# Kernel tuning notes

Measured on AMD Instinct MI355X. Metric: run time of the kernel, lower is better.

Reference implementation:

```python
import jax, jax.numpy as jnp
import numpy as np

# Lattice / model constants (from init_kwargs)
LX, LY = 12, 12
N = LX * LY
NH = 64              # GRU hidden units
K = 2                # local Hilbert-space dim (occupied / empty)
NSAMPLES = 4096
EPS = 1e-10


def setup_inputs() -> dict:
    key = jax.random.key(0)
    k1, k2, k3 = jax.random.split(key, 3)
    s_in = 1.0 / np.sqrt(K + NH)   # glorot-ish scale for input kernel
    s_rec = 1.0 / np.sqrt(NH)
    W = (jax.random.normal(k1, (K, 3 * NH)) * s_in).astype(jnp.float32)    # GRU input kernel
    U = (jax.random.normal(k2, (NH, 3 * NH)) * s_rec).astype(jnp.float32)  # GRU recurrent kernel
    b = jnp.zeros((2, 3 * NH), dtype=jnp.float32)   # reset_after: [input_bias, recurrent_bias]
    Wd = (jax.random.normal(k3, (NH, K)) * s_rec).astype(jnp.float32)      # Dense kernel
    bd = jnp.zeros((K,), dtype=jnp.float32)
    return {"nsamples": NSAMPLES, "W": W, "U": U, "b": b, "Wd": Wd, "bd": bd}


def _gru_cell(x, h, W, U, b):
    # TF2 Keras GRU cell, reset_after=True, tanh / sigmoid activations.
    xm = x @ W + b[0]                      # [ns, 3nh]
    hm = h @ U + b[1]                      # [ns, 3nh]
    xz, xr, xn = jnp.split(xm, 3, axis=1)
    hz, hr, hn = jnp.split(hm, 3, axis=1)
    z = jax.nn.sigmoid(xz + hz)            # update gate
    r = jax.nn.sigmoid(xr + hr)            # reset gate
    hh = jnp.tanh(xn + r * hn)             # candidate
    return z * h + (1.0 - z) * hh


def reference(nsamples, W, U, b, Wd, bd):
    keys = jax.random.split(jax.random.key(42), N)
    h0 = jnp.zeros((nsamples, NH), dtype=W.dtype)
    x0 = jnp.zeros((nsamples, K), dtype=W.dtype)   # 0.0 * one_hot(0)
    logP0 = jnp.zeros((nsamples,), dtype=W.dtype)

    def step(carry, k):
        h, x, logP = carry
        h = _gru_cell(x, h, W, U, b)
        probs = jax.nn.softmax(h @ Wd + bd, axis=-1)     # Dense with softmax activation
        logp = jnp.log(EPS + probs)                      # [ns, K]
        s = jax.random.categorical(k, logp, axis=-1)     # [ns] int sample
        x_new = jax.nn.one_hot(s, K, dtype=W.dtype)
        logP = logP + jnp.sum(logp * x_new, axis=1)
        return (h, x_new, logP), s

    (_, _, logP), samples = jax.lax.scan(step, (h0, x0, logP0), keys)
    samples = samples.T                                  # [ns, N]
    return samples, logP
```

## Files before the change

### kernel.cpp

```cpp
#include <hip/hip_runtime.h>
#include <cstdint>
#include <math.h>


#define NSAMP 4096
#define NSTEP 144
#define HID 64
#define CPB 2

typedef float v16f __attribute__((ext_vector_type(16)));
typedef float v4f  __attribute__((ext_vector_type(4)));
typedef float v2f  __attribute__((ext_vector_type(2)));

__device__ __forceinline__ void threefry2x32(uint32_t k0, uint32_t k1,
                                             uint32_t x0, uint32_t x1,
                                             uint32_t& o0, uint32_t& o1) {
  const uint32_t ks0 = k0, ks1 = k1, ks2 = k0 ^ k1 ^ 0x1BD11BDAu;
  x0 += ks0; x1 += ks1;
#define TF_ROUND(d) { x0 += x1; x1 = (x1 << (d)) | (x1 >> (32 - (d))); x1 ^= x0; }
  TF_ROUND(13) TF_ROUND(15) TF_ROUND(26) TF_ROUND(6)
  x0 += ks1; x1 += ks2 + 1u;
  TF_ROUND(17) TF_ROUND(29) TF_ROUND(16) TF_ROUND(24)
  x0 += ks2; x1 += ks0 + 2u;
  TF_ROUND(13) TF_ROUND(15) TF_ROUND(26) TF_ROUND(6)
  x0 += ks0; x1 += ks1 + 3u;
  TF_ROUND(17) TF_ROUND(29) TF_ROUND(16) TF_ROUND(24)
  x0 += ks1; x1 += ks2 + 4u;
  TF_ROUND(13) TF_ROUND(15) TF_ROUND(26) TF_ROUND(6)
  x0 += ks2; x1 += ks0 + 5u;
#undef TF_ROUND
  o0 = x0; o1 = x1;
}

__device__ __forceinline__ float fsig(float x) {
  return __builtin_amdgcn_rcpf(1.0f + __expf(-x));
}
__device__ __forceinline__ float ftanh(float x) {
  const float e = __expf(2.0f * x);
  return 1.0f - 2.0f * __builtin_amdgcn_rcpf(e + 1.0f);
}

#define PKFMA_LO(acc, h2, up) \
  asm("v_pk_fma_f32 %0, %1, %2, %0 op_sel_hi:[1,0,1]" \
      : "+v"(acc) : "v"(h2), "v"(up));
#define PKFMA_HI(acc, h2, up) \
  asm("v_pk_fma_f32 %0, %1, %2, %0 op_sel:[0,1,0] op_sel_hi:[1,1,1]" \
      : "+v"(acc) : "v"(h2), "v"(up));

template <int CTRL>
__device__ __forceinline__ float dpp_add(float v) {
  union { float f; int i; } c; c.f = v;
  union { int i; float f; } r;
  r.i = __builtin_amdgcn_mov_dpp(c.i, CTRL, 0xF, 0xF, true);
  return v + r.f;
}
#define DPP_XOR1 0xB1
#define DPP_XOR2 0x4E
#define DPP_XOR4 0x141
#define DPP_XOR8 0x140

__global__ __launch_bounds__(64, 1) void vmc_kernel(
    const float* __restrict__ W, const float* __restrict__ U,
    const float* __restrict__ B, const float* __restrict__ Wd,
    const float* __restrict__ Bd, float* __restrict__ out) {
  const int j = threadIdx.x;
  const int s_base = blockIdx.x * CPB;

  __shared__ __align__(16) float2 hsh2[HID];
  __shared__ uint2 kkeys[NSTEP];
  __shared__ float gsh[CPB * 2 * NSTEP];

#pragma unroll 1
  for (int t = j; t < NSTEP; t += HID) {
    uint32_t o0, o1;
    threefry2x32(0u, 42u, 0u, (uint32_t)t, o0, o1);
    kkeys[t].x = o0; kkeys[t].y = o1;
  }
  hsh2[j] = float2{0.0f, 0.0f};
  __syncthreads();

#pragma unroll 1
  for (int id = j; id < CPB * 2 * NSTEP; id += HID) {
    const int c = id / 288;
    const int idx = id - c * 288;
    const uint2 kt = kkeys[idx >> 1];
    const uint32_t i = 2u * (uint32_t)(s_base + c) + (uint32_t)(idx & 1);
    uint32_t o0, o1;
    threefry2x32(kt.x, kt.y, 0u, i, o0, o1);
    const uint32_t bits = o0 ^ o1;
    union { uint32_t u; float f; } cv; cv.u = (bits >> 9) | 0x3F800000u;
    float uf = cv.f - 1.0f;
    uf = fmaxf(uf, 1.17549435e-38f);
    const float inner = (float)log((double)uf);
    gsh[id] = -(float)log((double)(-inner));
  }
  __syncthreads();

  v16f uz0, uz1, uz2, uz3, ur0, ur1, ur2, ur3, un0, un1, un2, un3;
#define LOADB(v, r, off) \
  { _Pragma("unroll") for (int e = 0; e < 16; ++e) v[e] = U[((r)*16 + e)*192 + (off) + j]; }
  LOADB(uz0, 0, 0)    LOADB(uz1, 1, 0)    LOADB(uz2, 2, 0)    LOADB(uz3, 3, 0)
  LOADB(ur0, 0, 64)   LOADB(ur1, 1, 64)   LOADB(ur2, 2, 64)   LOADB(ur3, 3, 64)
  LOADB(un0, 0, 128)  LOADB(un1, 1, 128)  LOADB(un2, 2, 128)  LOADB(un3, 3, 128)
#undef LOADB

  const float b1z = B[192 + j], b1r = B[256 + j], b1n = B[320 + j];
  const float b0z = B[j],       b0r = B[64 + j],  b0n = B[128 + j];
  const float xW0z = W[j]       + b0z, xW1z = W[192 + j] + b0z;
  const float xW0r = W[64 + j]  + b0r, xW1r = W[256 + j] + b0r;
  const float xW0n = W[128 + j] + b0n, xW1n = W[320 + j] + b0n;
  const float wdd = Wd[2*j + 1] - Wd[2*j];
  const float bdd = Bd[1] - Bd[0];

  float ha = 0.0f, hb_ = 0.0f;
  float logPa = 0.0f, logPb = 0.0f;
  float axz = b0z, axr = b0r, axn = b0n;
  float bxz = b0z, bxr = b0r, bxn = b0n;
  v2f hz2 = {0.f, 0.f}, hr2 = {0.f, 0.f}, hn2 = {0.f, 0.f};

  for (int t = 0; t < NSTEP; ++t) {
    {
      const float az = axz + (hz2.x + b1z), ar = axr + (hr2.x + b1r);
      const float zz = fsig(az), rr = fsig(ar);
      const float hh = ftanh(axn + rr * (hn2.x + b1n));
      ha = zz * ha + (1.0f - zz) * hh;
    }
    {
      const float az = bxz + (hz2.y + b1z), ar = bxr + (hr2.y + b1r);
      const float zz = fsig(az), rr = fsig(ar);
      const float hh = ftanh(bxn + rr * (hn2.y + b1n));
      hb_ = zz * hb_ + (1.0f - zz) * hh;
    }
    hsh2[j] = float2{ha, hb_};

    float da = ha * wdd, db = hb_ * wdd;
    da = dpp_add<DPP_XOR1>(da); db = dpp_add<DPP_XOR1>(db);
    da = dpp_add<DPP_XOR2>(da); db = dpp_add<DPP_XOR2>(db);
    da = dpp_add<DPP_XOR4>(da); db = dpp_add<DPP_XOR4>(db);
    da = dpp_add<DPP_XOR8>(da); db = dpp_add<DPP_XOR8>(db);
    da += __shfl_xor(da, 16, 64); db += __shfl_xor(db, 16, 64);
    da += __shfl_xor(da, 32, 64); db += __shfl_xor(db, 32, 64);

    int sma, smb;
    {
      const float d = da + bdd;
      const float p1 = fsig(d), p0 = fsig(-d);
      const float lp0 = __logf(1e-10f + p0);
      const float lp1 = __logf(1e-10f + p1);
      const float g0 = gsh[2*t], g1 = gsh[2*t + 1];
      sma = (lp1 + g1) > (lp0 + g0);
      logPa += sma ? lp1 : lp0;
      axz = sma ? xW1z : xW0z;
      axr = sma ? xW1r : xW0r;
      axn = sma ? xW1n : xW0n;
    }
    {
      const float d = db + bdd;
      const float p1 = fsig(d), p0 = fsig(-d);
      const float lp0 = __logf(1e-10f + p0);
      const float lp1 = __logf(1e-10f + p1);
      const float g0 = gsh[288 + 2*t], g1 = gsh[288 + 2*t + 1];
      smb = (lp1 + g1) > (lp0 + g0);
      logPb += smb ? lp1 : lp0;
      bxz = smb ? xW1z : xW0z;
      bxr = smb ? xW1r : xW0r;
      bxn = smb ? xW1n : xW0n;
    }
    if (j == 0) {
      out[(s_base + 0) * NSTEP + t] = sma ? 1.0f : 0.0f;
      out[(s_base + 1) * NSTEP + t] = smb ? 1.0f : 0.0f;
    }

    hz2 = v2f{0.f, 0.f}; hr2 = v2f{0.f, 0.f}; hn2 = v2f{0.f, 0.f};
#define DOTC(uzv, urv, unv, blk, cc) \
    { const int c_ = (blk)*4 + (cc); \
      const v4f hA = *(const v4f*)&hsh2[c_*4]; \
      const v4f hB = *(const v4f*)&hsh2[c_*4 + 2]; \
      const v2f h0  = __builtin_shufflevector(hA, hA, 0, 1); \
      const v2f h1  = __builtin_shufflevector(hA, hA, 2, 3); \
      const v2f h2_ = __builtin_shufflevector(hB, hB, 0, 1); \
      const v2f h3  = __builtin_shufflevector(hB, hB, 2, 3); \
      const v2f uz01 = __builtin_shufflevector(uzv, uzv, (cc)*4 + 0, (cc)*4 + 1); \
      const v2f uz23 = __builtin_shufflevector(uzv, uzv, (cc)*4 + 2, (cc)*4 + 3); \
      const v2f ur01 = __builtin_shufflevector(urv, urv, (cc)*4 + 0, (cc)*4 + 1); \
      const v2f ur23 = __builtin_shufflevector(urv, urv, (cc)*4 + 2, (cc)*4 + 3); \
      const v2f un01 = __builtin_shufflevector(unv, unv, (cc)*4 + 0, (cc)*4 + 1); \
      const v2f un23 = __builtin_shufflevector(unv, unv, (cc)*4 + 2, (cc)*4 + 3); \
      PKFMA_LO(hz2, h0,  uz01) PKFMA_LO(hr2, h0,  ur01) PKFMA_LO(hn2, h0,  un01) \
      PKFMA_HI(hz2, h1,  uz01) PKFMA_HI(hr2, h1,  ur01) PKFMA_HI(hn2, h1,  un01) \
      PKFMA_LO(hz2, h2_, uz23) PKFMA_LO(hr2, h2_, ur23) PKFMA_LO(hn2, h2_, un23) \
      PKFMA_HI(hz2, h3,  uz23) PKFMA_HI(hr2, h3,  ur23) PKFMA_HI(hn2, h3,  un23) }
#define DOTBLK(uzv, urv, unv, blk) \
    DOTC(uzv, urv, unv, blk, 0) DOTC(uzv, urv, unv, blk, 1) \
    DOTC(uzv, urv, unv, blk, 2) DOTC(uzv, urv, unv, blk, 3)
    DOTBLK(uz0, ur0, un0, 0)
    DOTBLK(uz1, ur1, un1, 1)
    DOTBLK(uz2, ur2, un2, 2)
    DOTBLK(uz3, ur3, un3, 3)
#undef DOTBLK
#undef DOTC
  }

  if (j == 0) {
    *(float2*)&out[NSAMP * NSTEP + s_base] = float2{logPa, logPb};
  }
}

extern "C" void kernel_launch(void* const* d_in, const int* in_sizes, int n_in,
                              void* d_out, int out_size, void* d_ws, size_t ws_size,
                              hipStream_t stream) {
  const float* W  = (const float*)d_in[1];
  const float* U  = (const float*)d_in[2];
  const float* B  = (const float*)d_in[3];
  const float* Wd = (const float*)d_in[4];
  const float* Bd = (const float*)d_in[5];
  vmc_kernel<<<dim3(NSAMP / CPB), dim3(HID), 0, stream>>>(W, U, B, Wd, Bd, (float*)d_out);
}
```

Baseline: 301.6 us.

## Process four sample chains per wavefront to amortize register-resident U weights

Each 64-thread block now advances four independent sampling chains instead of two. The hidden states are stored as float4 in shared memory, and the packed FMAs reuse each U weight pair for two pairs of chains. This halves the block count and the per-chain cost of loading U into registers, and it gives more independent work to hide the latency of the serial reduce and sample chain. In exchange it adds accumulator registers and lengthens each step, and with 1024 blocks on a large GPU there may be too few waves to fill the machine.

Measured after the change: 371.3 us. 23.1% more time.

```diff
diff --git a/kernel.cpp b/kernel.cpp
--- a/kernel.cpp
+++ b/kernel.cpp
@@ -6,7 +6,7 @@
 #define NSAMP 4096
 #define NSTEP 144
 #define HID 64
-#define CPB 2
+#define CPW 4
 
 typedef float v16f __attribute__((ext_vector_type(16)));
 typedef float v4f  __attribute__((ext_vector_type(4)));
@@ -64,11 +64,11 @@
     const float* __restrict__ B, const float* __restrict__ Wd,
     const float* __restrict__ Bd, float* __restrict__ out) {
   const int j = threadIdx.x;
-  const int s_base = blockIdx.x * CPB;
-
-  __shared__ __align__(16) float2 hsh2[HID];
+  const int s_base = blockIdx.x * CPW;
+
+  __shared__ __align__(16) float4 hsh4[HID];
   __shared__ uint2 kkeys[NSTEP];
-  __shared__ float gsh[CPB * 2 * NSTEP];
+  __shared__ float gsh[CPW * 2 * NSTEP];
 
 #pragma unroll 1
   for (int t = j; t < NSTEP; t += HID) {
@@ -76,11 +76,11 @@
     threefry2x32(0u, 42u, 0u, (uint32_t)t, o0, o1);
     kkeys[t].x = o0; kkeys[t].y = o1;
   }
-  hsh2[j] = float2{0.0f, 0.0f};
+  hsh4[j] = float4{0.0f, 0.0f, 0.0f, 0.0f};
   __syncthreads();
 
 #pragma unroll 1
-  for (int id = j; id < CPB * 2 * NSTEP; id += HID) {
+  for (int id = j; id < CPW * 2 * NSTEP; id += HID) {
     const int c = id / 288;
     const int idx = id - c * 288;
     const uint2 kt = kkeys[idx >> 1];
@@ -112,84 +112,85 @@
   const float wdd = Wd[2*j + 1] - Wd[2*j];
   const float bdd = Bd[1] - Bd[0];
 
-  float ha = 0.0f, hb_ = 0.0f;
-  float logPa = 0.0f, logPb = 0.0f;
-  float axz = b0z, axr = b0r, axn = b0n;
-  float bxz = b0z, bxr = b0r, bxn = b0n;
-  v2f hz2 = {0.f, 0.f}, hr2 = {0.f, 0.f}, hn2 = {0.f, 0.f};
+  float hcur[CPW], logP[CPW], axz[CPW], axr[CPW], axn[CPW];
+#pragma unroll
+  for (int cc = 0; cc < CPW; ++cc) {
+    hcur[cc] = 0.0f; logP[cc] = 0.0f;
+    axz[cc] = b0z; axr[cc] = b0r; axn[cc] = b0n;
+  }
+  v2f hzAB = {0.f, 0.f}, hzCD = {0.f, 0.f};
+  v2f hrAB = {0.f, 0.f}, hrCD = {0.f, 0.f};
+  v2f hnAB = {0.f, 0.f}, hnCD = {0.f, 0.f};
 
   for (int t = 0; t < NSTEP; ++t) {
-    {
-      const float az = axz + (hz2.x + b1z), ar = axr + (hr2.x + b1r);
-      const float zz = fsig(az), rr = fsig(ar);
-      const float hh = ftanh(axn + rr * (hn2.x + b1n));
-      ha = zz * ha + (1.0f - zz) * hh;
+#define GATE(cc, hzv, hrv, hnv) { \
+      const float az = axz[cc] + ((hzv) + b1z), ar = axr[cc] + ((hrv) + b1r); \
+      const float zz = fsig(az), rr = fsig(ar); \
+      const float hh = ftanh(axn[cc] + rr * ((hnv) + b1n)); \
+      hcur[cc] = zz * hcur[cc] + (1.0f - zz) * hh; }
+    GATE(0, hzAB.x, hrAB.x, hnAB.x)
+    GATE(1, hzAB.y, hrAB.y, hnAB.y)
+    GATE(2, hzCD.x, hrCD.x, hnCD.x)
+    GATE(3, hzCD.y, hrCD.y, hnCD.y)
+#undef GATE
+    hsh4[j] = float4{hcur[0], hcur[1], hcur[2], hcur[3]};
+
+    int smv[CPW];
+#define CHAIN_DEC(cc) { \
+      float d_ = hcur[cc] * wdd; \
+      d_ = dpp_add<DPP_XOR1>(d_); d_ = dpp_add<DPP_XOR2>(d_); \
+      d_ = dpp_add<DPP_XOR4>(d_); d_ = dpp_add<DPP_XOR8>(d_); \
+      d_ += __shfl_xor(d_, 16, 64); d_ += __shfl_xor(d_, 32, 64); \
+      const float d = d_ + bdd; \
+      const float p1 = fsig(d), p0 = fsig(-d); \
+      const float lp0 = __logf(1e-10f + p0); \
+      const float lp1 = __logf(1e-10f + p1); \
+      const float g0 = gsh[(cc)*288 + 2*t], g1 = gsh[(cc)*288 + 2*t + 1]; \
+      const int sm = (lp1 + g1) > (lp0 + g0); \
+      logP[cc] += sm ? lp1 : lp0; \
+      axz[cc] = sm ? xW1z : xW0z; \
+      axr[cc] = sm ? xW1r : xW0r; \
+      axn[cc] = sm ? xW1n : xW0n; \
+      smv[cc] = sm; }
+    CHAIN_DEC(0) CHAIN_DEC(1) CHAIN_DEC(2) CHAIN_DEC(3)
+#undef CHAIN_DEC
+    if (j == 0) {
+      out[(s_base + 0) * NSTEP + t] = smv[0] ? 1.0f : 0.0f;
+      out[(s_base + 1) * NSTEP + t] = smv[1] ? 1.0f : 0.0f;
+      out[(s_base + 2) * NSTEP + t] = smv[2] ? 1.0f : 0.0f;
+      out[(s_base + 3) * NSTEP + t] = smv[3] ? 1.0f : 0.0f;
     }
-    {
-      const float az = bxz + (hz2.y + b1z), ar = bxr + (hr2.y + b1r);
-      const float zz = fsig(az), rr = fsig(ar);
-      const float hh = ftanh(bxn + rr * (hn2.y + b1n));
-      hb_ = zz * hb_ + (1.0f - zz) * hh;
-    }
-    hsh2[j] = float2{ha, hb_};
-
-    float da = ha * wdd, db = hb_ * wdd;
-    da = dpp_add<DPP_XOR1>(da); db = dpp_add<DPP_XOR1>(db);
-    da = dpp_add<DPP_XOR2>(da); db = dpp_add<DPP_XOR2>(db);
-    da = dpp_add<DPP_XOR4>(da); db = dpp_add<DPP_XOR4>(db);
-    da = dpp_add<DPP_XOR8>(da); db = dpp_add<DPP_XOR8>(db);
-    da += __shfl_xor(da, 16, 64); db += __shfl_xor(db, 16, 64);
-    da += __shfl_xor(da, 32, 64); db += __shfl_xor(db, 32, 64);
-
-    int sma, smb;
-    {
-      const float d = da + bdd;
-      const float p1 = fsig(d), p0 = fsig(-d);
-      const float lp0 = __logf(1e-10f + p0);
-      const float lp1 = __logf(1e-10f + p1);
-      const float g0 = gsh[2*t], g1 = gsh[2*t + 1];
-      sma = (lp1 + g1) > (lp0 + g0);
-      logPa += sma ? lp1 : lp0;
-      axz = sma ? xW1z : xW0z;
-      axr = sma ? xW1r : xW0r;
-      axn = sma ? xW1n : xW0n;
-    }
-    {
-      const float d = db + bdd;
-      const float p1 = fsig(d), p0 = fsig(-d);
-      const float lp0 = __logf(1e-10f + p0);
-      const float lp1 = __logf(1e-10f + p1);
-      const float g0 = gsh[288 + 2*t], g1 = gsh[288 + 2*t + 1];
-      smb = (lp1 + g1) > (lp0 + g0);
-      logPb += smb ? lp1 : lp0;
-      bxz = smb ? xW1z : xW0z;
-      bxr = smb ? xW1r : xW0r;
-      bxn = smb ? xW1n : xW0n;
-    }
-    if (j == 0) {
-      out[(s_base + 0) * NSTEP + t] = sma ? 1.0f : 0.0f;
-      out[(s_base + 1) * NSTEP + t] = smb ? 1.0f : 0.0f;
-    }
-
-    hz2 = v2f{0.f, 0.f}; hr2 = v2f{0.f, 0.f}; hn2 = v2f{0.f, 0.f};
+
+    hzAB = v2f{0.f, 0.f}; hzCD = v2f{0.f, 0.f};
+    hrAB = v2f{0.f, 0.f}; hrCD = v2f{0.f, 0.f};
+    hnAB = v2f{0.f, 0.f}; hnCD = v2f{0.f, 0.f};
+#define SV2(x, a, b) __builtin_shufflevector(x, x, a, b)
 #define DOTC(uzv, urv, unv, blk, cc) \
     { const int c_ = (blk)*4 + (cc); \
-      const v4f hA = *(const v4f*)&hsh2[c_*4]; \
-      const v4f hB = *(const v4f*)&hsh2[c_*4 + 2]; \
-      const v2f h0  = __builtin_shufflevector(hA, hA, 0, 1); \
-      const v2f h1  = __builtin_shufflevector(hA, hA, 2, 3); \
-      const v2f h2_ = __builtin_shufflevector(hB, hB, 0, 1); \
-      const v2f h3  = __builtin_shufflevector(hB, hB, 2, 3); \
-      const v2f uz01 = __builtin_shufflevector(uzv, uzv, (cc)*4 + 0, (cc)*4 + 1); \
-      const v2f uz23 = __builtin_shufflevector(uzv, uzv, (cc)*4 + 2, (cc)*4 + 3); \
-      const v2f ur01 = __builtin_shufflevector(urv, urv, (cc)*4 + 0, (cc)*4 + 1); \
-      const v2f ur23 = __builtin_shufflevector(urv, urv, (cc)*4 + 2, (cc)*4 + 3); \
-      const v2f un01 = __builtin_shufflevector(unv, unv, (cc)*4 + 0, (cc)*4 + 1); \
-      const v2f un23 = __builtin_shufflevector(unv, unv, (cc)*4 + 2, (cc)*4 + 3); \
-      PKFMA_LO(hz2, h0,  uz01) PKFMA_LO(hr2, h0,  ur01) PKFMA_LO(hn2, h0,  un01) \
-      PKFMA_HI(hz2, h1,  uz01) PKFMA_HI(hr2, h1,  ur01) PKFMA_HI(hn2, h1,  un01) \
-      PKFMA_LO(hz2, h2_, uz23) PKFMA_LO(hr2, h2_, ur23) PKFMA_LO(hn2, h2_, un23) \
-      PKFMA_HI(hz2, h3,  uz23) PKFMA_HI(hr2, h3,  ur23) PKFMA_HI(hn2, h3,  un23) }
+      const v4f h40 = *(const v4f*)&hsh4[c_*4 + 0]; \
+      const v4f h41 = *(const v4f*)&hsh4[c_*4 + 1]; \
+      const v4f h42 = *(const v4f*)&hsh4[c_*4 + 2]; \
+      const v4f h43 = *(const v4f*)&hsh4[c_*4 + 3]; \
+      const int e_ = (cc)*4; \
+      const v2f uz01 = SV2(uzv, e_+0, e_+1), uz23 = SV2(uzv, e_+2, e_+3); \
+      const v2f ur01 = SV2(urv, e_+0, e_+1), ur23 = SV2(urv, e_+2, e_+3); \
+      const v2f un01 = SV2(unv, e_+0, e_+1), un23 = SV2(unv, e_+2, e_+3); \
+      { const v2f hab = SV2(h40, 0, 1), hcd = SV2(h40, 2, 3); \
+        PKFMA_LO(hzAB, hab, uz01) PKFMA_LO(hzCD, hcd, uz01) \
+        PKFMA_LO(hrAB, hab, ur01) PKFMA_LO(hrCD, hcd, ur01) \
+        PKFMA_LO(hnAB, hab, un01) PKFMA_LO(hnCD, hcd, un01) } \
+      { const v2f hab = SV2(h41, 0, 1), hcd = SV2(h41, 2, 3); \
+        PKFMA_HI(hzAB, hab, uz01) PKFMA_HI(hzCD, hcd, uz01) \
+        PKFMA_HI(hrAB, hab, ur01) PKFMA_HI(hrCD, hcd, ur01) \
+        PKFMA_HI(hnAB, hab, un01) PKFMA_HI(hnCD, hcd, un01) } \
+      { const v2f hab = SV2(h42, 0, 1), hcd = SV2(h42, 2, 3); \
+        PKFMA_LO(hzAB, hab, uz23) PKFMA_LO(hzCD, hcd, uz23) \
+        PKFMA_LO(hrAB, hab, ur23) PKFMA_LO(hrCD, hcd, ur23) \
+        PKFMA_LO(hnAB, hab, un23) PKFMA_LO(hnCD, hcd, un23) } \
+      { const v2f hab = SV2(h43, 0, 1), hcd = SV2(h43, 2, 3); \
+        PKFMA_HI(hzAB, hab, uz23) PKFMA_HI(hzCD, hcd, uz23) \
+        PKFMA_HI(hrAB, hab, ur23) PKFMA_HI(hrCD, hcd, ur23) \
+        PKFMA_HI(hnAB, hab, un23) PKFMA_HI(hnCD, hcd, un23) } }
 #define DOTBLK(uzv, urv, unv, blk) \
     DOTC(uzv, urv, unv, blk, 0) DOTC(uzv, urv, unv, blk, 1) \
     DOTC(uzv, urv, unv, blk, 2) DOTC(uzv, urv, unv, blk, 3)
@@ -199,10 +200,12 @@
     DOTBLK(uz3, ur3, un3, 3)
 #undef DOTBLK
 #undef DOTC
+#undef SV2
   }
 
   if (j == 0) {
-    *(float2*)&out[NSAMP * NSTEP + s_base] = float2{logPa, logPb};
+    *(float4*)&out[NSAMP * NSTEP + s_base] =
+        make_float4(logP[0], logP[1], logP[2], logP[3]);
   }
 }
 
@@ -214,5 +217,6 @@
   const float* B  = (const float*)d_in[3];
   const float* Wd = (const float*)d_in[4];
   const float* Bd = (const float*)d_in[5];
-  vmc_kernel<<<dim3(NSAMP / CPB), dim3(HID), 0, stream>>>(W, U, B, Wd, Bd, (float*)d_out);
-}
+  vmc_kernel<<<dim3(NSAMP / CPW), dim3(HID), 0, stream>>>(
+      W, U, B, Wd, Bd, (float*)d_out);
+}
```
